# Optimization experiments

Measured on AMD Instinct MI355X. Metric: run time of the kernel, lower is better.

## Reference

```python
import jax, jax.numpy as jnp
import numpy as np

N = 4096                 # num nodes
SP, GE, TE = 256, 8, 64  # modality input dims
E = 32                   # embed_dim == hidden_features == out_features
H = 2                    # num_heads
D3 = 3 * E               # combined dim = 96
NEG_SLOPE = 0.2


def setup_inputs() -> dict:
    key = jax.random.key(0)
    ks = iter(jax.random.split(key, 64))
    nrm = lambda shape, s=0.05: jax.random.normal(next(ks), shape, jnp.float32) * s
    inp = {
        "spatial": jax.random.normal(next(ks), (N, SP), jnp.float32),
        "genomic": jax.random.normal(next(ks), (N, GE), jnp.float32),
        "temporal": jax.random.normal(next(ks), (N, TE), jnp.float32),
        "adj_matrix": jax.random.randint(next(ks), (N, N), 0, 2, jnp.int32),
        # modality embedding MLPs (Linear + LayerNorm)
        "sp_w": nrm((SP, E)), "sp_b": jnp.zeros((E,)), "sp_lg": jnp.ones((E,)), "sp_lb": jnp.zeros((E,)),
        "ge_w": nrm((GE, E)), "ge_b": jnp.zeros((E,)), "ge_lg": jnp.ones((E,)), "ge_lb": jnp.zeros((E,)),
        "te_w": nrm((TE, E)), "te_b": jnp.zeros((E,)), "te_lg": jnp.ones((E,)), "te_lb": jnp.zeros((E,)),
        # GAT: W_shared [96 -> H*E], attention vector a [2E], out_proj [H*E -> E], LayerNorm(E)
        "gat_w": nrm((D3, H * E)), "gat_a": nrm((2 * E,)),
        "gat_ow": nrm((H * E, E)), "gat_ob": jnp.zeros((E,)),
        "gat_lg": jnp.ones((E,)), "gat_lb": jnp.zeros((E,)),
        # MultiheadAttention (embed 96): packed qkv in_proj and out_proj
        "mha_iw": nrm((D3, 3 * D3)), "mha_ib": jnp.zeros((3 * D3,)),
        "mha_ow": nrm((D3, D3)), "mha_ob": jnp.zeros((D3,)),
        # motor tower
        "m1_w": nrm((D3, 2 * E)), "m1_b": jnp.zeros((2 * E,)), "m1_lg": jnp.ones((2 * E,)), "m1_lb": jnp.zeros((2 * E,)),
        "m2_w": nrm((2 * E, E)), "m2_b": jnp.zeros((E,)), "m2_lg": jnp.ones((E,)), "m2_lb": jnp.zeros((E,)),
        "m3_w": nrm((E, 1)), "m3_b": jnp.zeros((1,)),
        # cognitive tower
        "c1_w": nrm((D3, 2 * E)), "c1_b": jnp.zeros((2 * E,)), "c1_lg": jnp.ones((2 * E,)), "c1_lb": jnp.zeros((2 * E,)),
        "c2_w": nrm((2 * E, E)), "c2_b": jnp.zeros((E,)), "c2_lg": jnp.ones((E,)), "c2_lb": jnp.zeros((E,)),
        "c3_w": nrm((E, 1)), "c3_b": jnp.zeros((1,)),
    }
    return inp


def _ln(x, g, b, eps=1e-5):
    m = x.mean(-1, keepdims=True)
    v = ((x - m) ** 2).mean(-1, keepdims=True)
    return (x - m) / jnp.sqrt(v + eps) * g + b


def _embed(x, w, b, lg, lb):
    return jax.nn.relu(_ln(x @ w + b, lg, lb))  # dropout is identity in eval


def _tower(x, w1, b1, lg1, lb1, w2, b2, lg2, lb2, w3, b3):
    h = jax.nn.relu(_ln(x @ w1 + b1, lg1, lb1))
    h = jax.nn.relu(_ln(h @ w2 + b2, lg2, lb2))
    return h @ w3 + b3


def reference(spatial, genomic, temporal, adj_matrix,
              sp_w, sp_b, sp_lg, sp_lb, ge_w, ge_b, ge_lg, ge_lb,
              te_w, te_b, te_lg, te_lb,
              gat_w, gat_a, gat_ow, gat_ob, gat_lg, gat_lb,
              mha_iw, mha_ib, mha_ow, mha_ob,
              m1_w, m1_b, m1_lg, m1_lb, m2_w, m2_b, m2_lg, m2_lb, m3_w, m3_b,
              c1_w, c1_b, c1_lg, c1_lb, c2_w, c2_b, c2_lg, c2_lb, c3_w, c3_b):
    n = spatial.shape[0]
    s_emb = _embed(spatial, sp_w, sp_b, sp_lg, sp_lb)
    g_emb = _embed(genomic, ge_w, ge_b, ge_lg, ge_lb)
    t_emb = _embed(temporal, te_w, te_b, te_lg, te_lb)
    combined = jnp.concatenate([s_emb, g_emb, t_emb], axis=-1)  # [N, 96]

    # --- TaskSpecificGAT ---
    h = (combined @ gat_w).reshape(n, H, E)  # [N, H, E]
    # e[i,j] = leaky_relu(a . [h_i ; h_j]) = leaky_relu((h @ a1)_i + (h @ a2)_j)
    a1, a2 = gat_a[:E], gat_a[E:]
    f1 = jnp.einsum('nhd,d->nh', h, a1)  # source term
    f2 = jnp.einsum('nhd,d->nh', h, a2)  # target term
    e = jax.nn.leaky_relu(f1[:, None, :] + f2[None, :, :], NEG_SLOPE)  # [N, N, H]
    e = jnp.where(adj_matrix[:, :, None] == 0, -jnp.inf, e)
    alpha = jax.nn.softmax(e, axis=1)  # softmax over neighbors j
    h_out = jnp.einsum('ijh,jhd->ihd', alpha, h).reshape(n, H * E)  # [N, 64]
    gat_out = _ln(h_out @ gat_ow + gat_ob, gat_lg, gat_lb)  # [N, 32]

    # gat_expanded = cat([gat_out]*3) -> [N, 96], attn over seq_len=1
    gx = jnp.tile(gat_out, (1, 3))
    # MHA with a single key/query: softmax over one key == 1, so output = out_proj(v)
    v = gx @ mha_iw[:, 2 * D3:] + mha_ib[2 * D3:]
    attn_out = v @ mha_ow + mha_ob

    final = attn_out + combined
    motor = _tower(final, m1_w, m1_b, m1_lg, m1_lb, m2_w, m2_b, m2_lg, m2_lb, m3_w, m3_b)
    cognitive = jax.nn.sigmoid(
        _tower(final, c1_w, c1_b, c1_lg, c1_lb, c2_w, c2_b, c2_lg, c2_lb, c3_w, c3_b))
    return (motor, cognitive)
```

## Files before the change

kernel.cpp:

```cpp
#include <hip/hip_runtime.h>
#include <math.h>

#define NN 4096
#define LOG2E 1.4426950408889634f

typedef short short8 __attribute__((ext_vector_type(8)));
typedef float f32x4 __attribute__((ext_vector_type(4)));

#define OFF_COMB   0u
#define OFF_F1     393216u
#define OFF_F2     401408u
#define OFF_W2     409616u
#define OFF_B2     412688u
#define OFF_HT     412800u
#define OFF_PACK   543872u
#define OFF_PART   1068160u

__device__ inline unsigned short f2bf(float x) {
  unsigned u = __float_as_uint(x);
  unsigned r = u + 0x7FFFu + ((u >> 16) & 1u);
  return (unsigned short)(r >> 16);
}

__global__ __launch_bounds__(256) void k_pack(
    const int* __restrict__ adj, unsigned long long* __restrict__ pack)
{
  size_t t = (size_t)blockIdx.x * 256 + threadIdx.x;
  unsigned long long m = __ballot(adj[t] != 0);
  if ((threadIdx.x & 63) == 0) pack[t >> 6] = m;
}

__global__ __launch_bounds__(256) void k_comb(
    const float* __restrict__ spatial, const float* __restrict__ genomic,
    const float* __restrict__ temporal,
    const float* __restrict__ sp_w, const float* __restrict__ sp_b,
    const float* __restrict__ sp_lg, const float* __restrict__ sp_lb,
    const float* __restrict__ ge_w, const float* __restrict__ ge_b,
    const float* __restrict__ ge_lg, const float* __restrict__ ge_lb,
    const float* __restrict__ te_w, const float* __restrict__ te_b,
    const float* __restrict__ te_lg, const float* __restrict__ te_lb,
    const float* __restrict__ mha_iw, const float* __restrict__ mha_ib,
    const float* __restrict__ mha_ow, const float* __restrict__ mha_ob,
    float* __restrict__ ws)
{
  int t = threadIdx.x;
  int blk = blockIdx.x;

  if (blk >= 1536) {
    if (blk < 1548) {
      int idx = (blk - 1536) * 256 + t;
      int b = idx / 96, col = idx - b * 96;
      float acc = 0.f;
      for (int r = 0; r < 96; r++) {
        float fw = mha_iw[b * 288 + 192 + r]
                 + mha_iw[(b + 32) * 288 + 192 + r]
                 + mha_iw[(b + 64) * 288 + 192 + r];
        acc = fmaf(fw, mha_ow[r * 96 + col], acc);
      }
      ws[OFF_W2 + b * 96 + col] = acc;
    } else {
      if (t < 96) {
        float acc = mha_ob[t];
        for (int r = 0; r < 96; r++) acc = fmaf(mha_ib[192 + r], mha_ow[r * 96 + t], acc);
        ws[OFF_B2 + t] = acc;
      }
    }
    return;
  }

  int j = blk * 8 + (t >> 5);
  int grp = j >> 12;
  int row = j & 4095;
  int c = t & 31;

  float val;
  const float* lg;
  const float* lb;
  if (grp == 0) {
    const float* in = spatial + (size_t)row * 256;
    float a0 = 0.f, a1 = 0.f, a2 = 0.f, a3 = 0.f;
#pragma unroll 4
    for (int k = 0; k < 256; k += 4) {
      float4 x = *(const float4*)(in + k);
      a0 = fmaf(x.x, sp_w[(k)     * 32 + c], a0);
      a1 = fmaf(x.y, sp_w[(k + 1) * 32 + c], a1);
      a2 = fmaf(x.z, sp_w[(k + 2) * 32 + c], a2);
      a3 = fmaf(x.w, sp_w[(k + 3) * 32 + c], a3);
    }
    val = sp_b[c] + ((a0 + a1) + (a2 + a3));
    lg = sp_lg; lb = sp_lb;
  } else if (grp == 1) {
    const float* in = genomic + (size_t)row * 8;
    float4 x0 = *(const float4*)(in);
    float4 x1 = *(const float4*)(in + 4);
    float a0 = ge_b[c];
    a0 = fmaf(x0.x, ge_w[0 * 32 + c], a0);
    a0 = fmaf(x0.y, ge_w[1 * 32 + c], a0);
    a0 = fmaf(x0.z, ge_w[2 * 32 + c], a0);
    a0 = fmaf(x0.w, ge_w[3 * 32 + c], a0);
    a0 = fmaf(x1.x, ge_w[4 * 32 + c], a0);
    a0 = fmaf(x1.y, ge_w[5 * 32 + c], a0);
    a0 = fmaf(x1.z, ge_w[6 * 32 + c], a0);
    a0 = fmaf(x1.w, ge_w[7 * 32 + c], a0);
    val = a0;
    lg = ge_lg; lb = ge_lb;
  } else {
    const float* in = temporal + (size_t)row * 64;
    float a0 = 0.f, a1 = 0.f, a2 = 0.f, a3 = 0.f;
#pragma unroll 4
    for (int k = 0; k < 64; k += 4) {
      float4 x = *(const float4*)(in + k);
      a0 = fmaf(x.x, te_w[(k)     * 32 + c], a0);
      a1 = fmaf(x.y, te_w[(k + 1) * 32 + c], a1);
      a2 = fmaf(x.z, te_w[(k + 2) * 32 + c], a2);
      a3 = fmaf(x.w, te_w[(k + 3) * 32 + c], a3);
    }
    val = te_b[c] + ((a0 + a1) + (a2 + a3));
    lg = te_lg; lb = te_lb;
  }

  float s1 = val, s2 = val * val;
#pragma unroll
  for (int m = 1; m < 32; m <<= 1) {
    s1 += __shfl_xor(s1, m, 32);
    s2 += __shfl_xor(s2, m, 32);
  }
  float mean = s1 * (1.f / 32.f);
  float var  = s2 * (1.f / 32.f) - mean * mean;
  float y = fmaxf((val - mean) * rsqrtf(var + 1e-5f) * lg[c] + lb[c], 0.f);
  ws[OFF_COMB + (size_t)row * 96 + grp * 32 + c] = y;
}

__global__ __launch_bounds__(256) void k_proj(
    const float* __restrict__ gat_w, const float* __restrict__ gat_a,
    float* __restrict__ ws)
{
  __shared__ float h_s[4][64];
  int t = threadIdx.x;
  int w = t >> 6, d = t & 63;
  int row0 = blockIdx.x * 4;
  int row = row0 + w;

  const float* crow = ws + OFF_COMB + (size_t)row * 96;
  float a0 = 0.f, a1 = 0.f;
#pragma unroll 8
  for (int k = 0; k < 96; k += 2) {
    a0 = fmaf(crow[k],     gat_w[k * 64 + d],       a0);
    a1 = fmaf(crow[k + 1], gat_w[(k + 1) * 64 + d], a1);
  }
  float h = a0 + a1;

  int dc = d & 31;
  float p1 = h * gat_a[dc];
  float p2 = h * gat_a[32 + dc];
#pragma unroll
  for (int m = 1; m < 32; m <<= 1) {
    p1 += __shfl_xor(p1, m, 32);
    p2 += __shfl_xor(p2, m, 32);
  }
  if (dc == 0) {
    int head = d >> 5;
    ws[OFF_F1 + head * NN + row] = p1;
    ws[OFF_F2 + head * NN + row] = p2;
  }

  h_s[w][d] = h;
  __syncthreads();
  if (t < 64) {
    unsigned u0 = (unsigned)f2bf(h_s[0][t]) | ((unsigned)f2bf(h_s[1][t]) << 16);
    unsigned u1 = (unsigned)f2bf(h_s[2][t]) | ((unsigned)f2bf(h_s[3][t]) << 16);
    uint2 v; v.x = u0; v.y = u1;
    unsigned short* hT = (unsigned short*)(ws + OFF_HT);
    *(uint2*)(hT + (size_t)t * NN + row0) = v;
  }
}

template<int NSC>
__global__ __launch_bounds__(256) void k_gat5(
    const unsigned long long* __restrict__ pack,
    const unsigned short* __restrict__ hT,
    const float* __restrict__ f1h,
    const float* __restrict__ f2h,
    float* __restrict__ part,
    float* __restrict__ lpart)
{
  constexpr int SLICE = NN / NSC;
  int t = threadIdx.x;
  int lane = t & 63, wv = t >> 6;
  int quad = lane >> 4, mrow = lane & 15;
  int ib = blockIdx.x * 64 + wv * 16;
  int i_lane = ib + mrow;
  int jb = blockIdx.y * SLICE;

  float f1v0 = f1h[i_lane];
  float f1v1 = f1h[NN + i_lane];

  f32x4 acc00 = {0.f, 0.f, 0.f, 0.f};
  f32x4 acc01 = {0.f, 0.f, 0.f, 0.f};
  f32x4 acc10 = {0.f, 0.f, 0.f, 0.f};
  f32x4 acc11 = {0.f, 0.f, 0.f, 0.f};
  float ls0 = 0.f, ls1 = 0.f;

  const unsigned long long* prow = pack + ((size_t)i_lane << 6);

#pragma unroll
  for (int ti = 0; ti < SLICE / 64; ti++) {
    int jt = jb + ti * 64;
    unsigned long long qm = prow[jt >> 6];
    int jq0 = jt + quad * 8;
    int jq1 = jq0 + 32;
    float4 fa0 = *(const float4*)(f2h + jq0);
    float4 fb0 = *(const float4*)(f2h + jq0 + 4);
    float4 fa1 = *(const float4*)(f2h + jq1);
    float4 fb1 = *(const float4*)(f2h + jq1 + 4);
    float4 fc0 = *(const float4*)(f2h + NN + jq0);
    float4 fd0 = *(const float4*)(f2h + NN + jq0 + 4);
    float4 fc1 = *(const float4*)(f2h + NN + jq1);
    float4 fd1 = *(const float4*)(f2h + NN + jq1 + 4);
    short8 b00a = *(const short8*)(hT + (size_t)(mrow)      * NN + jq0);
    short8 b01a = *(const short8*)(hT + (size_t)(16 + mrow) * NN + jq0);
    short8 b10a = *(const short8*)(hT + (size_t)(32 + mrow) * NN + jq0);
    short8 b11a = *(const short8*)(hT + (size_t)(48 + mrow) * NN + jq0);
    short8 b00b = *(const short8*)(hT + (size_t)(mrow)      * NN + jq1);
    short8 b01b = *(const short8*)(hT + (size_t)(16 + mrow) * NN + jq1);
    short8 b10b = *(const short8*)(hT + (size_t)(32 + mrow) * NN + jq1);
    short8 b11b = *(const short8*)(hT + (size_t)(48 + mrow) * NN + jq1);

    {
      float f2a[8] = {fa0.x, fa0.y, fa0.z, fa0.w, fb0.x, fb0.y, fb0.z, fb0.w};
      float f2b[8] = {fc0.x, fc0.y, fc0.z, fc0.w, fd0.x, fd0.y, fd0.z, fd0.w};
      unsigned mbits = (unsigned)(qm >> (quad * 8)) ;
      union { short8 v; unsigned short u[8]; } a0, a1;
#pragma unroll
      for (int k = 0; k < 8; k++) {
        float e0 = f1v0 + f2a[k];
        float le0 = fmaxf(e0, 0.2f * e0);
        float w0 = __builtin_amdgcn_exp2f(le0 * LOG2E);
        float e1 = f1v1 + f2b[k];
        float le1 = fmaxf(e1, 0.2f * e1);
        float w1 = __builtin_amdgcn_exp2f(le1 * LOG2E);
        bool on = (mbits >> k) & 1u;
        w0 = on ? w0 : 0.f;
        w1 = on ? w1 : 0.f;
        ls0 += w0; ls1 += w1;
        a0.u[k] = f2bf(w0);
        a1.u[k] = f2bf(w1);
      }
      acc00 = __builtin_amdgcn_mfma_f32_16x16x32_bf16(a0.v, b00a, acc00, 0, 0, 0);
      acc01 = __builtin_amdgcn_mfma_f32_16x16x32_bf16(a0.v, b01a, acc01, 0, 0, 0);
      acc10 = __builtin_amdgcn_mfma_f32_16x16x32_bf16(a1.v, b10a, acc10, 0, 0, 0);
      acc11 = __builtin_amdgcn_mfma_f32_16x16x32_bf16(a1.v, b11a, acc11, 0, 0, 0);
    }
    {
      float f2a[8] = {fa1.x, fa1.y, fa1.z, fa1.w, fb1.x, fb1.y, fb1.z, fb1.w};
      float f2b[8] = {fc1.x, fc1.y, fc1.z, fc1.w, fd1.x, fd1.y, fd1.z, fd1.w};
      unsigned mbits = (unsigned)(qm >> (32 + quad * 8));
      union { short8 v; unsigned short u[8]; } a0, a1;
#pragma unroll
      for (int k = 0; k < 8; k++) {
        float e0 = f1v0 + f2a[k];
        float le0 = fmaxf(e0, 0.2f * e0);
        float w0 = __builtin_amdgcn_exp2f(le0 * LOG2E);
        float e1 = f1v1 + f2b[k];
        float le1 = fmaxf(e1, 0.2f * e1);
        float w1 = __builtin_amdgcn_exp2f(le1 * LOG2E);
        bool on = (mbits >> k) & 1u;
        w0 = on ? w0 : 0.f;
        w1 = on ? w1 : 0.f;
        ls0 += w0; ls1 += w1;
        a0.u[k] = f2bf(w0);
        a1.u[k] = f2bf(w1);
      }
      acc00 = __builtin_amdgcn_mfma_f32_16x16x32_bf16(a0.v, b00b, acc00, 0, 0, 0);
      acc01 = __builtin_amdgcn_mfma_f32_16x16x32_bf16(a0.v, b01b, acc01, 0, 0, 0);
      acc10 = __builtin_amdgcn_mfma_f32_16x16x32_bf16(a1.v, b10b, acc10, 0, 0, 0);
      acc11 = __builtin_amdgcn_mfma_f32_16x16x32_bf16(a1.v, b11b, acc11, 0, 0, 0);
    }
  }

  ls0 += __shfl_xor(ls0, 16); ls0 += __shfl_xor(ls0, 32);
  ls1 += __shfl_xor(ls1, 16); ls1 += __shfl_xor(ls1, 32);

  int slot = blockIdx.y;
#pragma unroll
  for (int r = 0; r < 4; r++) {
    int ig = ib + quad * 4 + r;
    float* p = part + (size_t)ig * (NSC * 64) + slot * 64;
    p[mrow]      = acc00[r];
    p[16 + mrow] = acc01[r];
    p[32 + mrow] = acc10[r];
    p[48 + mrow] = acc11[r];
  }
  if (lane < 16) {
    int ig = ib + lane;
    lpart[((size_t)ig * NSC + slot) * 2]     = ls0;
    lpart[((size_t)ig * NSC + slot) * 2 + 1] = ls1;
  }
}

template<int NSC>
__global__ __launch_bounds__(256) void k_post3(
    const float* __restrict__ gat_ow, const float* __restrict__ gat_ob,
    const float* __restrict__ gat_lg, const float* __restrict__ gat_lb,
    const float* __restrict__ m1_w, const float* __restrict__ m1_b,
    const float* __restrict__ m1_lg, const float* __restrict__ m1_lb,
    const float* __restrict__ m2_w, const float* __restrict__ m2_b,
    const float* __restrict__ m2_lg, const float* __restrict__ m2_lb,
    const float* __restrict__ m3_w, const float* __restrict__ m3_b,
    const float* __restrict__ c1_w, const float* __restrict__ c1_b,
    const float* __restrict__ c1_lg, const float* __restrict__ c1_lb,
    const float* __restrict__ c2_w, const float* __restrict__ c2_b,
    const float* __restrict__ c2_lg, const float* __restrict__ c2_lb,
    const float* __restrict__ c3_w, const float* __restrict__ c3_b,
    const float* __restrict__ part, const float* __restrict__ lpart,
    const float* __restrict__ comb, const float* __restrict__ W2,
    const float* __restrict__ B2,
    float* __restrict__ out)
{
  int t = threadIdx.x;
  int w = t >> 6, l = t & 63;
  int i = blockIdx.x * 4 + w;

  __shared__ float sh_h[4][64];
  __shared__ float sh_go[4][32];
  __shared__ float sh_fin[4][96];
  __shared__ float sh_t1[4][2][64];

  {
    const float* pr = part + (size_t)i * (NSC * 64);
    float a0 = 0.f, a1 = 0.f, a2 = 0.f, a3 = 0.f;
#pragma unroll
    for (int s = 0; s < NSC; s += 4) {
      a0 += pr[(s)     * 64 + l];
      a1 += pr[(s + 1) * 64 + l];
      a2 += pr[(s + 2) * 64 + l];
      a3 += pr[(s + 3) * 64 + l];
    }
    float a = (a0 + a1) + (a2 + a3);
    const float* lr = lpart + (size_t)i * NSC * 2;
    float l0 = 0.f, l1 = 0.f;
#pragma unroll
    for (int s = 0; s < NSC; s++) { l0 += lr[s * 2]; l1 += lr[s * 2 + 1]; }
    sh_h[w][l] = a / (l < 32 ? l0 : l1);
  }
  __syncthreads();

  if (l < 32) {
    float acc = gat_ob[l];
#pragma unroll 8
    for (int r = 0; r < 64; r++) acc = fmaf(sh_h[w][r], gat_ow[r * 32 + l], acc);
    float s1 = acc, s2 = acc * acc;
#pragma unroll
    for (int m = 1; m < 32; m <<= 1) {
      s1 += __shfl_xor(s1, m, 32);
      s2 += __shfl_xor(s2, m, 32);
    }
    float mean = s1 * (1.f / 32.f), var = s2 * (1.f / 32.f) - mean * mean;
    sh_go[w][l] = (acc - mean) * rsqrtf(var + 1e-5f) * gat_lg[l] + gat_lb[l];
  }
  __syncthreads();

  {
    float accA = B2[l];
#pragma unroll 8
    for (int d = 0; d < 32; d++) accA = fmaf(sh_go[w][d], W2[d * 96 + l], accA);
    sh_fin[w][l] = accA + comb[(size_t)i * 96 + l];
    if (l < 32) {
      float accB = B2[64 + l];
#pragma unroll 8
      for (int d = 0; d < 32; d++) accB = fmaf(sh_go[w][d], W2[d * 96 + 64 + l], accB);
      sh_fin[w][64 + l] = accB + comb[(size_t)i * 96 + 64 + l];
    }
  }
  __syncthreads();

  {
    float am = m1_b[l], ac = c1_b[l];
#pragma unroll 4
    for (int r = 0; r < 96; r++) {
      float f = sh_fin[w][r];
      am = fmaf(f, m1_w[r * 64 + l], am);
      ac = fmaf(f, c1_w[r * 64 + l], ac);
    }
    float s1 = am, s2 = am * am;
#pragma unroll
    for (int m = 1; m < 64; m <<= 1) { s1 += __shfl_xor(s1, m); s2 += __shfl_xor(s2, m); }
    float mean = s1 * (1.f / 64.f), var = s2 * (1.f / 64.f) - mean * mean;
    sh_t1[w][0][l] = fmaxf((am - mean) * rsqrtf(var + 1e-5f) * m1_lg[l] + m1_lb[l], 0.f);
    s1 = ac; s2 = ac * ac;
#pragma unroll
    for (int m = 1; m < 64; m <<= 1) { s1 += __shfl_xor(s1, m); s2 += __shfl_xor(s2, m); }
    mean = s1 * (1.f / 64.f); var = s2 * (1.f / 64.f) - mean * mean;
    sh_t1[w][1][l] = fmaxf((ac - mean) * rsqrtf(var + 1e-5f) * c1_lg[l] + c1_lb[l], 0.f);
  }
  __syncthreads();

  {
    int tw = l >> 5, c = l & 31;
    const float* w2  = tw ? c2_w  : m2_w;
    const float* b2  = tw ? c2_b  : m2_b;
    const float* lg2 = tw ? c2_lg : m2_lg;
    const float* lb2 = tw ? c2_lb : m2_lb;
    float a2 = b2[c];
#pragma unroll 4
    for (int r = 0; r < 64; r++) a2 = fmaf(sh_t1[w][tw][r], w2[r * 32 + c], a2);
    float u1 = a2, u2 = a2 * a2;
#pragma unroll
    for (int m = 1; m < 32; m <<= 1) {
      u1 += __shfl_xor(u1, m, 32);
      u2 += __shfl_xor(u2, m, 32);
    }
    float mean = u1 * (1.f / 32.f), var = u2 * (1.f / 32.f) - mean * mean;
    float y2 = fmaxf((a2 - mean) * rsqrtf(var + 1e-5f) * lg2[c] + lb2[c], 0.f);
    float p = y2 * (tw ? c3_w[c] : m3_w[c]);
#pragma unroll
    for (int m = 1; m < 32; m <<= 1) p += __shfl_xor(p, m, 32);
    if (c == 0) {
      float v = p + (tw ? c3_b[0] : m3_b[0]);
      if (tw) out[NN + i] = 1.f / (1.f + expf(-v));
      else    out[i] = v;
    }
  }
}

extern "C" void kernel_launch(void* const* d_in, const int* in_sizes, int n_in,
                              void* d_out, int out_size, void* d_ws, size_t ws_size,
                              hipStream_t stream) {
  (void)in_sizes; (void)n_in; (void)out_size;
  const float* spatial  = (const float*)d_in[0];
  const float* genomic  = (const float*)d_in[1];
  const float* temporal = (const float*)d_in[2];
  const int*   adj      = (const int*)d_in[3];
  const float* sp_w = (const float*)d_in[4];
  const float* sp_b = (const float*)d_in[5];
  const float* sp_lg = (const float*)d_in[6];
  const float* sp_lb = (const float*)d_in[7];
  const float* ge_w = (const float*)d_in[8];
  const float* ge_b = (const float*)d_in[9];
  const float* ge_lg = (const float*)d_in[10];
  const float* ge_lb = (const float*)d_in[11];
  const float* te_w = (const float*)d_in[12];
  const float* te_b = (const float*)d_in[13];
  const float* te_lg = (const float*)d_in[14];
  const float* te_lb = (const float*)d_in[15];
  const float* gat_w = (const float*)d_in[16];
  const float* gat_a = (const float*)d_in[17];
  const float* gat_ow = (const float*)d_in[18];
  const float* gat_ob = (const float*)d_in[19];
  const float* gat_lg = (const float*)d_in[20];
  const float* gat_lb = (const float*)d_in[21];
  const float* mha_iw = (const float*)d_in[22];
  const float* mha_ib = (const float*)d_in[23];
  const float* mha_ow = (const float*)d_in[24];
  const float* mha_ob = (const float*)d_in[25];
  const float* m1_w = (const float*)d_in[26];
  const float* m1_b = (const float*)d_in[27];
  const float* m1_lg = (const float*)d_in[28];
  const float* m1_lb = (const float*)d_in[29];
  const float* m2_w = (const float*)d_in[30];
  const float* m2_b = (const float*)d_in[31];
  const float* m2_lg = (const float*)d_in[32];
  const float* m2_lb = (const float*)d_in[33];
  const float* m3_w = (const float*)d_in[34];
  const float* m3_b = (const float*)d_in[35];
  const float* c1_w = (const float*)d_in[36];
  const float* c1_b = (const float*)d_in[37];
  const float* c1_lg = (const float*)d_in[38];
  const float* c1_lb = (const float*)d_in[39];
  const float* c2_w = (const float*)d_in[40];
  const float* c2_b = (const float*)d_in[41];
  const float* c2_lg = (const float*)d_in[42];
  const float* c2_lb = (const float*)d_in[43];
  const float* c3_w = (const float*)d_in[44];
  const float* c3_b = (const float*)d_in[45];

  float* ws  = (float*)d_ws;
  float* out = (float*)d_out;
  float* part = ws + OFF_PART;

  k_pack<<<(NN * NN) / 256, 256, 0, stream>>>(adj, (unsigned long long*)(ws + OFF_PACK));
  k_comb<<<1549, 256, 0, stream>>>(spatial, genomic, temporal,
                                   sp_w, sp_b, sp_lg, sp_lb,
                                   ge_w, ge_b, ge_lg, ge_lb,
                                   te_w, te_b, te_lg, te_lb,
                                   mha_iw, mha_ib, mha_ow, mha_ob, ws);
  k_proj<<<NN / 4, 256, 0, stream>>>(gat_w, gat_a, ws);

  size_t need16 = (size_t)(OFF_PART + 16ul * NN * 64 + 16ul * NN * 2) * 4;
  if (ws_size >= need16) {
    float* lpart = part + 16ul * NN * 64;
    dim3 g2(NN / 64, 16);
    k_gat5<16><<<g2, 256, 0, stream>>>((const unsigned long long*)(ws + OFF_PACK),
                                       (const unsigned short*)(ws + OFF_HT),
                                       ws + OFF_F1, ws + OFF_F2, part, lpart);
    k_post3<16><<<NN / 4, 256, 0, stream>>>(gat_ow, gat_ob, gat_lg, gat_lb,
                                            m1_w, m1_b, m1_lg, m1_lb,
                                            m2_w, m2_b, m2_lg, m2_lb,
                                            m3_w, m3_b,
                                            c1_w, c1_b, c1_lg, c1_lb,
                                            c2_w, c2_b, c2_lg, c2_lb,
                                            c3_w, c3_b,
                                            part, lpart, ws + OFF_COMB,
                                            ws + OFF_W2, ws + OFF_B2, out);
  } else {
    float* lpart = part + 8ul * NN * 64;
    dim3 g2(NN / 64, 8);
    k_gat5<8><<<g2, 256, 0, stream>>>((const unsigned long long*)(ws + OFF_PACK),
                                      (const unsigned short*)(ws + OFF_HT),
                                      ws + OFF_F1, ws + OFF_F2, part, lpart);
    k_post3<8><<<NN / 4, 256, 0, stream>>>(gat_ow, gat_ob, gat_lg, gat_lb,
                                           m1_w, m1_b, m1_lg, m1_lb,
                                           m2_w, m2_b, m2_lg, m2_lb,
                                           m3_w, m3_b,
                                           c1_w, c1_b, c1_lg, c1_lb,
                                           c2_w, c2_b, c2_lg, c2_lb,
                                           c3_w, c3_b,
                                           part, lpart, ws + OFF_COMB,
                                           ws + OFF_W2, ws + OFF_B2, out);
  }
}
```

Before: 271.5 us.

## Fuse adjacency bit-packing into GAT kernel and pre-swizzle hT for MFMA loads

Removes the separate k_pack pass. The GAT kernel now reads the int32 adjacency rows directly and builds each lane's 64-bit mask with 16 ballots per tile, saving one full write and read of the packed mask. A new k_repack kernel reorders the bf16 hT into MFMA-fragment order, so each B operand becomes one contiguous 16-byte load per lane. LOG2E is folded into f1/f2 at the projection stage, and the bf16 rounding is simplified to round-half-up. The cost is more ballot and adjacency load work inside the main kernel, and a slightly different rounding mode.

Result: faster. 241.2 us (median of 2 runs) (-11.2%).

```diff
diff --git a/kernel.cpp b/kernel.cpp
--- a/kernel.cpp
+++ b/kernel.cpp
@@ -13,21 +13,12 @@
 #define OFF_W2     409616u
 #define OFF_B2     412688u
 #define OFF_HT     412800u
-#define OFF_PACK   543872u
-#define OFF_PART   1068160u
+#define OFF_HT2    543872u
+#define OFF_PART   674944u
 
 __device__ inline unsigned short f2bf(float x) {
   unsigned u = __float_as_uint(x);
-  unsigned r = u + 0x7FFFu + ((u >> 16) & 1u);
-  return (unsigned short)(r >> 16);
-}
-
-__global__ __launch_bounds__(256) void k_pack(
-    const int* __restrict__ adj, unsigned long long* __restrict__ pack)
-{
-  size_t t = (size_t)blockIdx.x * 256 + threadIdx.x;
-  unsigned long long m = __ballot(adj[t] != 0);
-  if ((threadIdx.x & 63) == 0) pack[t >> 6] = m;
+  return (unsigned short)((u + 0x8000u) >> 16);
 }
 
 __global__ __launch_bounds__(256) void k_comb(
@@ -160,8 +151,8 @@
   }
   if (dc == 0) {
     int head = d >> 5;
-    ws[OFF_F1 + head * NN + row] = p1;
-    ws[OFF_F2 + head * NN + row] = p2;
+    ws[OFF_F1 + head * NN + row] = p1 * LOG2E;
+    ws[OFF_F2 + head * NN + row] = p2 * LOG2E;
   }
 
   h_s[w][d] = h;
@@ -175,10 +166,27 @@
   }
 }
 
+__global__ __launch_bounds__(256) void k_repack(float* __restrict__ ws)
+{
+  const unsigned short* hT = (const unsigned short*)(ws + OFF_HT);
+  unsigned short* hT2 = (unsigned short*)(ws + OFF_HT2);
+  int R = blockIdx.x * 256 + threadIdx.x;
+  int T = R >> 9;
+  int r = R & 511;
+  int c = r >> 8;
+  int g = (r >> 6) & 3;
+  int l = r & 63;
+  int quad = l >> 4, mrow = l & 15;
+  int j0 = T * 64 + c * 32 + quad * 8;
+  int d  = g * 16 + mrow;
+  short8 v = *(const short8*)(hT + (size_t)d * NN + j0);
+  *(short8*)(hT2 + (size_t)R * 8) = v;
+}
+
 template<int NSC>
-__global__ __launch_bounds__(256) void k_gat5(
-    const unsigned long long* __restrict__ pack,
-    const unsigned short* __restrict__ hT,
+__global__ __launch_bounds__(256) void k_gat6(
+    const int* __restrict__ adj,
+    const unsigned short* __restrict__ hT2,
     const float* __restrict__ f1h,
     const float* __restrict__ f2h,
     float* __restrict__ part,
@@ -201,12 +209,30 @@
   f32x4 acc11 = {0.f, 0.f, 0.f, 0.f};
   float ls0 = 0.f, ls1 = 0.f;
 
-  const unsigned long long* prow = pack + ((size_t)i_lane << 6);
+  const int* adjT = adj + (size_t)ib * NN;
 
 #pragma unroll
   for (int ti = 0; ti < SLICE / 64; ti++) {
     int jt = jb + ti * 64;
-    unsigned long long qm = prow[jt >> 6];
+
+    unsigned long long qm = 0;
+#pragma unroll
+    for (int r = 0; r < 16; r++) {
+      int av = adjT[(size_t)r * NN + jt + lane];
+      unsigned long long b = __ballot(av != 0);
+      if (mrow == r) qm = b;
+    }
+
+    const unsigned short* hb = hT2 + ((size_t)(jt >> 6)) * 4096;
+    short8 b00a = *(const short8*)(hb + (0 * 4 + 0) * 512 + lane * 8);
+    short8 b01a = *(const short8*)(hb + (0 * 4 + 1) * 512 + lane * 8);
+    short8 b10a = *(const short8*)(hb + (0 * 4 + 2) * 512 + lane * 8);
+    short8 b11a = *(const short8*)(hb + (0 * 4 + 3) * 512 + lane * 8);
+    short8 b00b = *(const short8*)(hb + (1 * 4 + 0) * 512 + lane * 8);
+    short8 b01b = *(const short8*)(hb + (1 * 4 + 1) * 512 + lane * 8);
+    short8 b10b = *(const short8*)(hb + (1 * 4 + 2) * 512 + lane * 8);
+    short8 b11b = *(const short8*)(hb + (1 * 4 + 3) * 512 + lane * 8);
+
     int jq0 = jt + quad * 8;
     int jq1 = jq0 + 32;
     float4 fa0 = *(const float4*)(f2h + jq0);
@@ -217,28 +243,18 @@
     float4 fd0 = *(const float4*)(f2h + NN + jq0 + 4);
     float4 fc1 = *(const float4*)(f2h + NN + jq1);
     float4 fd1 = *(const float4*)(f2h + NN + jq1 + 4);
-    short8 b00a = *(const short8*)(hT + (size_t)(mrow)      * NN + jq0);
-    short8 b01a = *(const short8*)(hT + (size_t)(16 + mrow) * NN + jq0);
-    short8 b10a = *(const short8*)(hT + (size_t)(32 + mrow) * NN + jq0);
-    short8 b11a = *(const short8*)(hT + (size_t)(48 + mrow) * NN + jq0);
-    short8 b00b = *(const short8*)(hT + (size_t)(mrow)      * NN + jq1);
-    short8 b01b = *(const short8*)(hT + (size_t)(16 + mrow) * NN + jq1);
-    short8 b10b = *(const short8*)(hT + (size_t)(32 + mrow) * NN + jq1);
-    short8 b11b = *(const short8*)(hT + (size_t)(48 + mrow) * NN + jq1);
 
     {
       float f2a[8] = {fa0.x, fa0.y, fa0.z, fa0.w, fb0.x, fb0.y, fb0.z, fb0.w};
       float f2b[8] = {fc0.x, fc0.y, fc0.z, fc0.w, fd0.x, fd0.y, fd0.z, fd0.w};
-      unsigned mbits = (unsigned)(qm >> (quad * 8)) ;
+      unsigned mbits = (unsigned)(qm >> (quad * 8));
       union { short8 v; unsigned short u[8]; } a0, a1;
 #pragma unroll
       for (int k = 0; k < 8; k++) {
         float e0 = f1v0 + f2a[k];
-        float le0 = fmaxf(e0, 0.2f * e0);
-        float w0 = __builtin_amdgcn_exp2f(le0 * LOG2E);
+        float w0 = __builtin_amdgcn_exp2f(fmaxf(e0, 0.2f * e0));
         float e1 = f1v1 + f2b[k];
-        float le1 = fmaxf(e1, 0.2f * e1);
-        float w1 = __builtin_amdgcn_exp2f(le1 * LOG2E);
+        float w1 = __builtin_amdgcn_exp2f(fmaxf(e1, 0.2f * e1));
         bool on = (mbits >> k) & 1u;
         w0 = on ? w0 : 0.f;
         w1 = on ? w1 : 0.f;
@@ -259,11 +275,9 @@
 #pragma unroll
       for (int k = 0; k < 8; k++) {
         float e0 = f1v0 + f2a[k];
-        float le0 = fmaxf(e0, 0.2f * e0);
-        float w0 = __builtin_amdgcn_exp2f(le0 * LOG2E);
+        float w0 = __builtin_amdgcn_exp2f(fmaxf(e0, 0.2f * e0));
         float e1 = f1v1 + f2b[k];
-        float le1 = fmaxf(e1, 0.2f * e1);
-        float w1 = __builtin_amdgcn_exp2f(le1 * LOG2E);
+        float w1 = __builtin_amdgcn_exp2f(fmaxf(e1, 0.2f * e1));
         bool on = (mbits >> k) & 1u;
         w0 = on ? w0 : 0.f;
         w1 = on ? w1 : 0.f;
@@ -478,20 +492,20 @@
   float* out = (float*)d_out;
   float* part = ws + OFF_PART;
 
-  k_pack<<<(NN * NN) / 256, 256, 0, stream>>>(adj, (unsigned long long*)(ws + OFF_PACK));
   k_comb<<<1549, 256, 0, stream>>>(spatial, genomic, temporal,
                                    sp_w, sp_b, sp_lg, sp_lb,
                                    ge_w, ge_b, ge_lg, ge_lb,
                                    te_w, te_b, te_lg, te_lb,
                                    mha_iw, mha_ib, mha_ow, mha_ob, ws);
   k_proj<<<NN / 4, 256, 0, stream>>>(gat_w, gat_a, ws);
+  k_repack<<<128, 256, 0, stream>>>(ws);
 
   size_t need16 = (size_t)(OFF_PART + 16ul * NN * 64 + 16ul * NN * 2) * 4;
   if (ws_size >= need16) {
     float* lpart = part + 16ul * NN * 64;
     dim3 g2(NN / 64, 16);
-    k_gat5<16><<<g2, 256, 0, stream>>>((const unsigned long long*)(ws + OFF_PACK),
-                                       (const unsigned short*)(ws + OFF_HT),
+    k_gat6<16><<<g2, 256, 0, stream>>>(adj,
+                                       (const unsigned short*)(ws + OFF_HT2),
                                        ws + OFF_F1, ws + OFF_F2, part, lpart);
     k_post3<16><<<NN / 4, 256, 0, stream>>>(gat_ow, gat_ob, gat_lg, gat_lb,
                                             m1_w, m1_b, m1_lg, m1_lb,
@@ -505,8 +519,8 @@
   } else {
     float* lpart = part + 8ul * NN * 64;
     dim3 g2(NN / 64, 8);
-    k_gat5<8><<<g2, 256, 0, stream>>>((const unsigned long long*)(ws + OFF_PACK),
-                                      (const unsigned short*)(ws + OFF_HT),
+    k_gat6<8><<<g2, 256, 0, stream>>>(adj,
+                                      (const unsigned short*)(ws + OFF_HT2),
                                       ws + OFF_F1, ws + OFF_F2, part, lpart);
     k_post3<8><<<NN / 4, 256, 0, stream>>>(gat_ow, gat_ob, gat_lg, gat_lb,
                                            m1_w, m1_b, m1_lg, m1_lb,
```
